# Optimization experiments

Hardware: AMD Instinct MI355X
Metric: run time of the kernel (lower is better)

The kernel has to match this reference:

```python
import jax, jax.numpy as jnp
import numpy as np

K_TOP = 2
NUM_HEADS = 8
NOISE_EPS = 0.01
GATE_EPS = 1e-9
LOSS_COEF = 0.01


def _xavier(key, shape):
    fan_in, fan_out = shape[-2], shape[-1]
    lim = float(np.sqrt(6.0 / (fan_in + fan_out)))
    return jax.random.uniform(key, shape, jnp.float32, -lim, lim)


def setup_inputs():
    key = jax.random.key(0)
    ks = jax.random.split(key, 12)
    B, S, D, E = 32, 512, 512, 8
    return {
        "q": jax.random.normal(ks[0], (B, S, D), jnp.float32),
        "k": jax.random.normal(ks[1], (B, S, D), jnp.float32),
        "v": jax.random.normal(ks[2], (B, S, D), jnp.float32),
        "mask": jnp.ones((1, 1, S, S), jnp.int32),
        "w_gate": _xavier(ks[3], (D, E)),
        "w_noise": _xavier(ks[4], (D, E)),
        "Wq": _xavier(ks[5], (E, D, D)),
        "bq": jnp.zeros((E, D), jnp.float32),
        "Wk": _xavier(ks[6], (E, D, D)),
        "bk": jnp.zeros((E, D), jnp.float32),
        "Wv": _xavier(ks[7], (E, D, D)),
        "bv": jnp.zeros((E, D), jnp.float32),
        "Wo": _xavier(ks[8], (E, D, D)),
        "bo": jnp.zeros((E, D), jnp.float32),
    }


def _cv_squared(x):
    # torch .var() is unbiased (ddof=1)
    return jnp.var(x, ddof=1) / (jnp.mean(x) ** 2 + 1e-10)


def _moe_attention(q, k, v, mask, w_gate, w_noise, Wq, bq, Wk, bk, Wv, bv, Wo, bo):
    B, S, D = q.shape
    E = w_gate.shape[1]
    H = NUM_HEADS
    dh = D // H

    # x[x != x] = 0 (in-place nan scrub of q, used for gating AND as query)
    qc = jnp.where(jnp.isnan(q), jnp.zeros((), q.dtype), q)

    # noisy top-k gating; the python loop sum_i x[:,i,:] @ W == x.sum(1) @ W
    xs = qc.sum(axis=1)                                  # [B, D]
    clean_logits = xs @ w_gate                           # [B, E]
    raw_noise = xs @ w_noise
    noise_std = jax.nn.softplus(raw_noise) + NOISE_EPS   # train=True
    noise = jax.random.normal(jax.random.key(42), clean_logits.shape, clean_logits.dtype)
    noisy_logits = clean_logits + noise * noise_std

    top_logits, top_idx = jax.lax.top_k(noisy_logits, K_TOP + 1)  # [B, k+1]
    tk_logits = top_logits[:, :K_TOP]
    tk_idx = top_idx[:, :K_TOP]                          # [B, k]
    tk_gates = jax.nn.softmax(tk_logits, axis=1) + GATE_EPS
    gates = jnp.zeros((B, E), clean_logits.dtype).at[jnp.arange(B)[:, None], tk_idx].set(tk_gates)

    # load via prob-in-top-k (noisy_gating and k < num_experts)
    thr_in = top_logits[:, K_TOP][:, None]
    thr_out = top_logits[:, K_TOP - 1][:, None]
    is_in = noisy_logits > thr_in
    cdf = jax.scipy.stats.norm.cdf
    prob = jnp.where(is_in, cdf((clean_logits - thr_in) / noise_std),
                     cdf((clean_logits - thr_out) / noise_std))
    load = prob.sum(axis=0)
    importance = gates.sum(axis=0)
    loss = (_cv_squared(importance) + _cv_squared(load)) * LOSS_COEF

    # sparse dispatch == per (batch, slot) run the selected expert's MHA.
    # Gather expert weights per selected slot: [B, k, D, D].
    def proj(x, W, b):
        return jnp.einsum('bsd,bjdf->bjsf', x, W[tk_idx]) + b[tk_idx][:, :, None, :]

    Q = proj(qc, Wq, bq).reshape(B, K_TOP, S, H, dh)
    Kx = proj(k, Wk, bk).reshape(B, K_TOP, S, H, dh)
    V = proj(v, Wv, bv).reshape(B, K_TOP, S, H, dh)

    scale = jnp.asarray(1.0 / np.sqrt(dh), q.dtype)
    scores = jnp.einsum('bjqhd,bjkhd->bjhqk', Q, Kx) * scale   # [B,k,H,S,S]
    m = mask[:, None]                                          # [1,1,1,S,S]
    scores = jnp.where(m == 0, jnp.asarray(-1e9, scores.dtype), scores)
    attn = jax.nn.softmax(scores, axis=-1)
    ctx = jnp.einsum('bjhqk,bjkhd->bjqhd', attn, V).reshape(B, K_TOP, S, D)
    out_e = jnp.einsum('bjsd,bjdf->bjsf', ctx, Wo[tk_idx]) + bo[tk_idx][:, :, None, :]

    # combine: sum_j gate * exp(out), clamp zeros to eps, log
    combined = jnp.einsum('bj,bjsd->bsd', tk_gates, jnp.exp(out_e))
    eps = jnp.asarray(np.finfo(np.float64).eps, combined.dtype)
    combined = jnp.where(combined == 0, eps, combined)
    return jnp.log(combined), loss


def reference(q, k, v, mask, w_gate, w_noise, Wq, bq, Wk, bk, Wv, bv, Wo, bo):
    return _moe_attention(q, k, v, mask, w_gate, w_noise, Wq, bq, Wk, bk, Wv, bv, Wo, bo)
```

## Files before the change

### kernel.cpp

```cpp
#include <hip/hip_runtime.h>
#include <math.h>

typedef unsigned int u32;
typedef unsigned long long u64;
typedef unsigned short u16t;

#define SD   512
#define EE   8
#define DH   64
#define SDSQ (512*512)
#define LDSW 72

typedef __attribute__((ext_vector_type(8))) short bfrag8;
typedef __attribute__((ext_vector_type(4))) float f32x4;
typedef __attribute__((ext_vector_type(8))) unsigned short u16x8;

typedef const __attribute__((address_space(1))) void gas_void;
typedef __attribute__((address_space(3))) void las_void;

#define MFMA_B16(a,b,c) __builtin_amdgcn_mfma_f32_16x16x32_bf16((a),(b),(c),0,0,0)

__device__ __forceinline__ u32 rotl32(u32 x, int r){ return (x<<r)|(x>>(32-r)); }

__device__ __forceinline__ u16t bf_hi(float a){
  u32 x; __builtin_memcpy(&x,&a,4);
  u32 r = x + 0x7fffu + ((x>>16)&1u);
  return (u16t)(r>>16);
}
__device__ __forceinline__ float bf_f(u16t h){
  u32 x = ((u32)h)<<16; float f; __builtin_memcpy(&f,&x,4); return f;
}
__device__ __forceinline__ void split2(float a, u16t& h, u16t& l){
  h = bf_hi(a);
  l = bf_hi(a - bf_f(h));
}

__device__ __forceinline__ void gload16(const u16t* g, u16t* l){
  __builtin_amdgcn_global_load_lds((gas_void*)g, (las_void*)l, 16, 0, 0);
}

__device__ __forceinline__ void threefry_0_42(u32 x0, u32 x1, u32& o0, u32& o1){
  const u32 k0=0u, k1=42u;
  const u32 ks2 = k0 ^ k1 ^ 0x1BD11BDAu;
  const int R0[4]={13,15,26,6}, R1[4]={17,29,16,24};
  x0 += k0; x1 += k1;
  #pragma unroll
  for(int r=0;r<4;r++){ x0+=x1; x1=rotl32(x1,R0[r]); x1^=x0; }
  x0+=k1; x1+=ks2+1u;
  #pragma unroll
  for(int r=0;r<4;r++){ x0+=x1; x1=rotl32(x1,R1[r]); x1^=x0; }
  x0+=ks2; x1+=k0+2u;
  #pragma unroll
  for(int r=0;r<4;r++){ x0+=x1; x1=rotl32(x1,R0[r]); x1^=x0; }
  x0+=k0; x1+=k1+3u;
  #pragma unroll
  for(int r=0;r<4;r++){ x0+=x1; x1=rotl32(x1,R1[r]); x1^=x0; }
  x0+=k1; x1+=ks2+4u;
  #pragma unroll
  for(int r=0;r<4;r++){ x0+=x1; x1=rotl32(x1,R0[r]); x1^=x0; }
  x0+=ks2; x1+=k0+5u;
  o0 = x0; o1 = x1;
}

__device__ double erfinv64(double x){
  double w = -log((1.0 - x) * (1.0 + x));
  double p;
  if (w < 5.0){
    w = w - 2.5;
    p = 2.81022636e-08;
    p = 3.43273939e-07 + p*w;
    p = -3.5233877e-06 + p*w;
    p = -4.39150654e-06 + p*w;
    p = 0.00021858087  + p*w;
    p = -0.00125372503 + p*w;
    p = -0.00417768164 + p*w;
    p = 0.246640727    + p*w;
    p = 1.50140941     + p*w;
  } else {
    w = sqrt(w) - 3.0;
    p = -0.000200214257;
    p = 0.000100950558 + p*w;
    p = 0.00134934322  + p*w;
    p = -0.00367342844 + p*w;
    p = 0.00573950773  + p*w;
    p = -0.0076224613  + p*w;
    p = 0.00943887047  + p*w;
    p = 1.00167406     + p*w;
    p = 2.83297682     + p*w;
  }
  double r = p * x;
  #pragma unroll
  for (int it=0; it<2; ++it){
    double e = erf(r) - x;
    r -= e / (1.1283791670955126 * exp(-r*r));
  }
  return r;
}

__device__ double jax_noise_part32(int i){
  u32 o0, o1;
  threefry_0_42(0u, (u32)i, o0, o1);
  u32 bits = o0 ^ o1;
  u32 fb = (bits >> 9) | 0x3f800000u;
  float f; __builtin_memcpy(&f, &fb, 4);
  f -= 1.0f;
  u32 lob = 0xBF7FFFFFu;
  float lo; __builtin_memcpy(&lo, &lob, 4);
  float t = f * 2.0f;
  float u = t + lo;
  u = fmaxf(u, lo);
  return 1.4142135623730951 * erfinv64((double)u);
}

__global__ __launch_bounds__(256) void k_cvt_x(
  const float* __restrict__ src, u16t* __restrict__ dh, u16t* __restrict__ dl, int clean)
{
  const int n4 = 32*SDSQ/4;
  int i = blockIdx.x*256 + threadIdx.x;
  if (i >= n4) return;
  float4 r = ((const float4*)src)[i];
  float a[4] = {r.x, r.y, r.z, r.w};
  if (clean){
    #pragma unroll
    for (int u=0;u<4;u++) if (isnan(a[u])) a[u] = 0.f;
  }
  u16t h[4], l[4];
  #pragma unroll
  for (int u=0;u<4;u++) split2(a[u], h[u], l[u]);
  ((ushort4*)dh)[i] = make_ushort4(h[0],h[1],h[2],h[3]);
  ((ushort4*)dl)[i] = make_ushort4(l[0],l[1],l[2],l[3]);
}

__global__ __launch_bounds__(256) void k_cvt_w(
  const float* __restrict__ W, u16t* __restrict__ th, u16t* __restrict__ tl)
{
  __shared__ u16t Th[64*LDSW], Tl[64*LDSW];
  int e = blockIdx.z;
  int k0 = blockIdx.y*64, f0 = blockIdx.x*64;
  int tid = threadIdx.x;
  int r = tid>>2, c4 = (tid&3)*16;
  const float* Wp = W + (size_t)e*SDSQ + (size_t)(k0+r)*SD + f0 + c4;
  #pragma unroll
  for (int i=0;i<4;i++){
    float4 rv = *(const float4*)(Wp + 4*i);
    float a[4]={rv.x,rv.y,rv.z,rv.w};
    #pragma unroll
    for (int u=0;u<4;u++){
      u16t h,l; split2(a[u],h,l);
      Th[(c4+4*i+u)*LDSW + r] = h;
      Tl[(c4+4*i+u)*LDSW + r] = l;
    }
  }
  __syncthreads();
  u16t* dh = th + (size_t)e*SDSQ + (size_t)(f0+r)*SD + k0 + c4;
  u16t* dl = tl + (size_t)e*SDSQ + (size_t)(f0+r)*SD + k0 + c4;
  *(u16x8*)dh     = *(const u16x8*)&Th[r*LDSW + c4];
  *(u16x8*)(dh+8) = *(const u16x8*)&Th[r*LDSW + c4 + 8];
  *(u16x8*)dl     = *(const u16x8*)&Tl[r*LDSW + c4];
  *(u16x8*)(dl+8) = *(const u16x8*)&Tl[r*LDSW + c4 + 8];
}

__global__ void k_xs(const float* __restrict__ q, double* __restrict__ xs){
  int b = blockIdx.x, d = threadIdx.x;
  const float* p = q + (size_t)b*SDSQ + d;
  double acc = 0.0;
  for (int s=0; s<SD; ++s){
    float f = p[(size_t)s*SD];
    if (!isnan(f)) acc += (double)f;
  }
  xs[b*SD + d] = acc;
}

__global__ __launch_bounds__(256) void k_gate(
    const double* __restrict__ xs, const float* __restrict__ wg,
    const float* __restrict__ wn, int* __restrict__ tk_idx,
    float* __restrict__ tk_gates, float* __restrict__ out_loss)
{
  __shared__ double cl_s[256], sd_s[256], nz_s[256], pr_s[256];
  __shared__ double thrI_s[32], thrO_s[32], g0_s[32], g1_s[32];
  __shared__ int i0_s[32], i1_s[32];
  int tid = threadIdx.x;
  int b = tid >> 3, e = tid & 7;
  double c=0.0, n=0.0;
  const double* xr = xs + b*SD;
  for (int d=0; d<SD; ++d){
    double x = xr[d];
    c += x * (double)wg[d*EE + e];
    n += x * (double)wn[d*EE + e];
  }
  double sp = fmax(n, 0.0) + log1p(exp(-fabs(n)));
  double sdv = sp + 0.01;
  double nz = c + jax_noise_part32(tid) * sdv;
  cl_s[tid]=c; sd_s[tid]=sdv; nz_s[tid]=nz;
  __syncthreads();
  if (tid < 32){
    int bb = tid;
    double v0=-INFINITY,v1=-INFINITY,v2=-INFINITY; int i0=0,i1=0;
    for (int ee=0; ee<8; ++ee){
      double vv = nz_s[bb*8+ee];
      if (vv > v0){ v2=v1; v1=v0;i1=i0; v0=vv;i0=ee; }
      else if (vv > v1){ v2=v1; v1=vv;i1=ee; }
      else if (vv > v2){ v2=vv; }
    }
    double e1 = exp(v1 - v0);
    double s = 1.0 + e1;
    double g0 = 1.0/s + 1e-9, g1 = e1/s + 1e-9;
    tk_idx[bb*2+0]=i0; tk_idx[bb*2+1]=i1;
    tk_gates[bb*2+0]=(float)g0; tk_gates[bb*2+1]=(float)g1;
    i0_s[bb]=i0; i1_s[bb]=i1; g0_s[bb]=g0; g1_s[bb]=g1;
    thrI_s[bb]=v2; thrO_s[bb]=v1;
  }
  __syncthreads();
  {
    double thrI = thrI_s[b], thrO = thrO_s[b];
    bool isin = nz_s[tid] > thrI;
    double t = (cl_s[tid] - (isin ? thrI : thrO)) / sd_s[tid];
    pr_s[tid] = 0.5 * (1.0 + erf(t * 0.7071067811865476));
  }
  __syncthreads();
  if (tid == 0){
    double imp[8], ld[8];
    for (int i=0;i<8;i++){ imp[i]=0.0; ld[i]=0.0; }
    for (int bb=0; bb<32; ++bb){
      imp[i0_s[bb]] += g0_s[bb];
      imp[i1_s[bb]] += g1_s[bb];
    }
    for (int i=0;i<256;i++) ld[i&7] += pr_s[i];
    double loss = 0.0;
    for (int a=0;a<2;a++){
      double* arr = a ? ld : imp;
      double mu=0.0; for(int i=0;i<8;i++) mu += arr[i]; mu *= 0.125;
      double var=0.0; for(int i=0;i<8;i++){ double dd=arr[i]-mu; var += dd*dd; }
      var *= (1.0/7.0);
      loss += var / (mu*mu + 1e-10);
    }
    loss *= 0.01;
    out_loss[0] = (float)loss;
  }
}

__global__ __launch_bounds__(256) void k_proj(
  const u16t* __restrict__ qh, const u16t* __restrict__ ql,
  const u16t* __restrict__ kh, const u16t* __restrict__ kl,
  const u16t* __restrict__ vh, const u16t* __restrict__ vl,
  const u16t* __restrict__ wqh, const u16t* __restrict__ wql,
  const u16t* __restrict__ wkh, const u16t* __restrict__ wkl,
  const u16t* __restrict__ wvh, const u16t* __restrict__ wvl,
  const float* __restrict__ bq, const float* __restrict__ bk, const float* __restrict__ bv,
  const int* __restrict__ tk_idx, int pair0,
  u16t* __restrict__ Qh, u16t* __restrict__ Ql,
  u16t* __restrict__ Kh, u16t* __restrict__ Kl,
  u16t* __restrict__ Vth, u16t* __restrict__ Vtl)
{
  __shared__ __align__(16) u16t SM[4*128*64];
  int z = blockIdx.z;
  int lp = z/3, m = z - lp*3;
  int gp = pair0 + lp;
  int b = gp >> 1;
  int e = tk_idx[gp] & 7;
  const u16t *Xh, *Xl, *Wh, *Wl; const float* bias; u16t *Yh, *Yl;
  if (m==0){ Xh=qh; Xl=ql; Wh=wqh; Wl=wql; bias=bq; Yh=Qh;  Yl=Ql;  }
  else if (m==1){ Xh=kh; Xl=kl; Wh=wkh; Wl=wkl; bias=bk; Yh=Kh;  Yl=Kl;  }
  else { Xh=vh; Xl=vl; Wh=wvh; Wl=wvl; bias=bv; Yh=Vth; Yl=Vtl; }
  bool tr = (m==2);
  Xh += (size_t)b*SDSQ; Xl += (size_t)b*SDSQ;
  Wh += (size_t)e*SDSQ; Wl += (size_t)e*SDSQ;
  bias += e*SD;
  Yh += (size_t)lp*SDSQ; Yl += (size_t)lp*SDSQ;

  int tid = threadIdx.x, w = tid>>6, lane = tid&63;
  int q16 = lane&15, quad = lane>>4;
  int wm = w>>1, wnn = w&1;
  int s0 = blockIdx.y*128, f0 = blockIdx.x*128;
  int row8 = lane>>3, cc = lane&7;
  int soff = (cc ^ row8)*8;
  int sw = q16 & 7;
  int aH_off = tr ? 16384 : 0;
  int bH_off = tr ? 0 : 16384;

  f32x4 acc[4][4];
  #pragma unroll
  for (int i=0;i<4;i++)
    #pragma unroll
    for (int j=0;j<4;j++) acc[i][j] = (f32x4){0.f,0.f,0.f,0.f};

  for (int k0=0;k0<SD;k0+=64){
    #pragma unroll
    for (int t=0;t<4;t++){
      int br = w*32 + t*8;
      int gr = br + row8;
      size_t ga  = (size_t)(s0+gr)*SD + k0 + soff;
      size_t gbo = (size_t)(f0+gr)*SD + k0 + soff;
      gload16(Xh + ga,  &SM[0     + br*64]);
      gload16(Xl + ga,  &SM[8192  + br*64]);
      gload16(Wh + gbo, &SM[16384 + br*64]);
      gload16(Wl + gbo, &SM[24576 + br*64]);
    }
    __syncthreads();
    #pragma unroll
    for (int kk=0;kk<2;kk++){
      int ch = kk*4 + quad;
      int co = (ch ^ sw)*8;
      bfrag8 fAH[4], fAL[4], fBH[4], fBL[4];
      #pragma unroll
      for (int i=0;i<4;i++){
        int ra = wm*64  + i*16 + q16;
        int rb = wnn*64 + i*16 + q16;
        fAH[i] = *(const bfrag8*)&SM[aH_off        + ra*64 + co];
        fAL[i] = *(const bfrag8*)&SM[aH_off + 8192 + ra*64 + co];
        fBH[i] = *(const bfrag8*)&SM[bH_off        + rb*64 + co];
        fBL[i] = *(const bfrag8*)&SM[bH_off + 8192 + rb*64 + co];
      }
      #pragma unroll
      for (int i=0;i<4;i++)
        #pragma unroll
        for (int j=0;j<4;j++){
          acc[i][j] = MFMA_B16(fAH[i], fBH[j], acc[i][j]);
          acc[i][j] = MFMA_B16(fAH[i], fBL[j], acc[i][j]);
          acc[i][j] = MFMA_B16(fAL[i], fBH[j], acc[i][j]);
        }
    }
    __syncthreads();
  }
  if (!tr){
    #pragma unroll
    for (int i=0;i<4;i++){
      #pragma unroll
      for (int j=0;j<4;j++){
        int f = f0 + wnn*64 + j*16 + q16;
        float bb = bias[f];
        #pragma unroll
        for (int rr=0;rr<4;rr++){
          int s = s0 + wm*64 + i*16 + quad*4 + rr;
          u16t hh, ll; split2(acc[i][j][rr] + bb, hh, ll);
          size_t o = (size_t)s*SD + f;
          Yh[o] = hh; Yl[o] = ll;
        }
      }
    }
  } else {
    #pragma unroll
    for (int i=0;i<4;i++){
      #pragma unroll
      for (int rr=0;rr<4;rr++){
        int fr = f0 + wm*64 + i*16 + quad*4 + rr;
        float bb = bias[fr];
        #pragma unroll
        for (int j=0;j<4;j++){
          int scol = s0 + wnn*64 + j*16 + q16;
          u16t hh, ll; split2(acc[i][j][rr] + bb, hh, ll);
          size_t o = (size_t)fr*SD + scol;
          Yh[o] = hh; Yl[o] = ll;
        }
      }
    }
  }
}

__global__ __launch_bounds__(256) void k_attn(
  const u16t* __restrict__ Qh, const u16t* __restrict__ Ql,
  const u16t* __restrict__ Kh, const u16t* __restrict__ Kl,
  const u16t* __restrict__ Vth, const u16t* __restrict__ Vtl,
  u16t* __restrict__ Ch, u16t* __restrict__ Cl)
{
  __shared__ __align__(16) u16t QH[64*64], QL[64*64];
  __shared__ __align__(16) u16t KH[64*64], KL[64*64];
  __shared__ __align__(16) u16t VTH[64*64], VTL[64*64];
  __shared__ __align__(16) u16t PS[64*LDSW];
  int lp = blockIdx.z, h = blockIdx.y, qt = blockIdx.x;
  int tid = threadIdx.x;
  int w = tid>>6, lane = tid&63, q16 = lane&15, quad = lane>>4;
  int s0 = qt*64;
  const size_t base  = (size_t)lp*SDSQ + h*DH;
  const size_t vbase = (size_t)lp*SDSQ + (size_t)h*DH*SD;
  int row8 = lane>>3, cc = lane&7;
  int soff = (cc ^ row8)*8;
  int sw = q16 & 7;

  #pragma unroll
  for (int t=0;t<2;t++){
    int br = w*16 + t*8, gr = br + row8;
    size_t ga = base + (size_t)(s0+gr)*SD + soff;
    gload16(Qh + ga, &QH[br*64]);
    gload16(Ql + ga, &QL[br*64]);
  }

  float m_row[4], l_row[4];
  f32x4 ctx[4];
  #pragma unroll
  for (int rr=0;rr<4;rr++){ m_row[rr]=-INFINITY; l_row[rr]=0.f; }
  #pragma unroll
  for (int nt=0;nt<4;nt++) ctx[nt] = (f32x4){0.f,0.f,0.f,0.f};

  for (int kt=0; kt<8; ++kt){
    #pragma unroll
    for (int t=0;t<2;t++){
      int br = w*16 + t*8, gr = br + row8;
      size_t gk = base + (size_t)(kt*64+gr)*SD + soff;
      gload16(Kh + gk, &KH[br*64]);
      gload16(Kl + gk, &KL[br*64]);
      size_t gv = vbase + (size_t)gr*SD + kt*64 + soff;
      gload16(Vth + gv, &VTH[br*64]);
      gload16(Vtl + gv, &VTL[br*64]);
    }
    __syncthreads();

    f32x4 sc[4];
    #pragma unroll
    for (int nt=0;nt<4;nt++) sc[nt] = (f32x4){0.f,0.f,0.f,0.f};
    #pragma unroll
    for (int kk=0;kk<2;kk++){
      int co = ((kk*4+quad) ^ sw)*8;
      bfrag8 aH = *(const bfrag8*)&QH[(w*16+q16)*64 + co];
      bfrag8 aL = *(const bfrag8*)&QL[(w*16+q16)*64 + co];
      #pragma unroll
      for (int nt=0;nt<4;nt++){
        bfrag8 bH = *(const bfrag8*)&KH[(nt*16+q16)*64 + co];
        bfrag8 bL = *(const bfrag8*)&KL[(nt*16+q16)*64 + co];
        sc[nt] = MFMA_B16(aH,bH,sc[nt]);
        sc[nt] = MFMA_B16(aH,bL,sc[nt]);
        sc[nt] = MFMA_B16(aL,bH,sc[nt]);
      }
    }
    #pragma unroll
    for (int nt=0;nt<4;nt++)
      #pragma unroll
      for (int rr=0;rr<4;rr++) sc[nt][rr] *= 0.125f;

    float alpha[4];
    #pragma unroll
    for (int rr=0;rr<4;rr++){
      float mx = sc[0][rr];
      #pragma unroll
      for (int nt=1;nt<4;nt++) mx = fmaxf(mx, sc[nt][rr]);
      mx = fmaxf(mx, __shfl_xor(mx, 1));
      mx = fmaxf(mx, __shfl_xor(mx, 2));
      mx = fmaxf(mx, __shfl_xor(mx, 4));
      mx = fmaxf(mx, __shfl_xor(mx, 8));
      float nm = fmaxf(m_row[rr], mx);
      alpha[rr] = expf(m_row[rr] - nm);
      m_row[rr] = nm;
    }
    #pragma unroll
    for (int rr=0;rr<4;rr++){
      float S = 0.f;
      #pragma unroll
      for (int nt=0;nt<4;nt++){
        float p = expf(sc[nt][rr] - m_row[rr]);
        sc[nt][rr] = p;
        S += p;
      }
      S += __shfl_xor(S, 1);
      S += __shfl_xor(S, 2);
      S += __shfl_xor(S, 4);
      S += __shfl_xor(S, 8);
      l_row[rr] = l_row[rr]*alpha[rr] + S;
      #pragma unroll
      for (int nt=0;nt<4;nt++) ctx[nt][rr] *= alpha[rr];
    }
    #pragma unroll
    for (int nt=0;nt<4;nt++)
      #pragma unroll
      for (int rr=0;rr<4;rr++)
        PS[(w*16 + quad*4 + rr)*LDSW + nt*16 + q16] = bf_hi(sc[nt][rr]);
    __syncthreads();

    #pragma unroll
    for (int kk2=0;kk2<2;kk2++){
      bfrag8 aP = *(const bfrag8*)&PS[(w*16+q16)*LDSW + kk2*32 + quad*8];
      int co2 = ((kk2*4+quad) ^ sw)*8;
      #pragma unroll
      for (int nt=0;nt<4;nt++){
        bfrag8 vH = *(const bfrag8*)&VTH[(nt*16+q16)*64 + co2];
        bfrag8 vL = *(const bfrag8*)&VTL[(nt*16+q16)*64 + co2];
        ctx[nt] = MFMA_B16(aP,vH,ctx[nt]);
        ctx[nt] = MFMA_B16(aP,vL,ctx[nt]);
      }
    }
    __syncthreads();
  }
  #pragma unroll
  for (int rr=0;rr<4;rr++){
    float inv = 1.f / l_row[rr];
    #pragma unroll
    for (int nt=0;nt<4;nt++){
      int s = s0 + w*16 + quad*4 + rr;
      u16t hh, ll; split2(ctx[nt][rr]*inv, hh, ll);
      size_t o = base + (size_t)s*SD + nt*16 + q16;
      Ch[o] = hh; Cl[o] = ll;
    }
  }
}

__global__ __launch_bounds__(256) void k_out(
  const u16t* __restrict__ Ch, const u16t* __restrict__ Cl,
  const u16t* __restrict__ Wth, const u16t* __restrict__ Wtl,
  const float* __restrict__ bo, const int* __restrict__ tk_idx,
  const float* __restrict__ tk_gates, int pair0, float* __restrict__ out)
{
  __shared__ __align__(16) u16t Ah[64*64], Al[64*64];
  __shared__ __align__(16) u16t Bh[64*64], Bl[64*64];
  int lb = blockIdx.z;
  int gb = (pair0 >> 1) + lb;
  int tid = threadIdx.x;
  int w = tid>>6, lane = tid&63, q16 = lane&15, quad = lane>>4;
  int s0 = blockIdx.y*64, f0 = blockIdx.x*64;
  int row8 = lane>>3, cc = lane&7;
  int soff = (cc ^ row8)*8;
  int sw = q16 & 7;

  f32x4 acc2[2][4];
  #pragma unroll
  for (int j=0;j<2;j++)
    #pragma unroll
    for (int nt=0;nt<4;nt++) acc2[j][nt] = (f32x4){0.f,0.f,0.f,0.f};

  for (int j=0;j<2;++j){
    int e = tk_idx[pair0 + lb*2 + j] & 7;
    const u16t* AH = Ch + (size_t)(lb*2+j)*SDSQ;
    const u16t* AL = Cl + (size_t)(lb*2+j)*SDSQ;
    const u16t* WH = Wth + (size_t)e*SDSQ;
    const u16t* WL = Wtl + (size_t)e*SDSQ;
    for (int k0=0;k0<SD;k0+=64){
      #pragma unroll
      for (int t=0;t<2;t++){
        int br = w*16 + t*8, gr = br + row8;
        size_t ga  = (size_t)(s0+gr)*SD + k0 + soff;
        size_t gbo = (size_t)(f0+gr)*SD + k0 + soff;
        gload16(AH + ga,  &Ah[br*64]);
        gload16(AL + ga,  &Al[br*64]);
        gload16(WH + gbo, &Bh[br*64]);
        gload16(WL + gbo, &Bl[br*64]);
      }
      __syncthreads();
      #pragma unroll
      for (int kk=0;kk<2;kk++){
        int co = ((kk*4+quad) ^ sw)*8;
        bfrag8 aH = *(const bfrag8*)&Ah[(w*16+q16)*64 + co];
        bfrag8 aL = *(const bfrag8*)&Al[(w*16+q16)*64 + co];
        #pragma unroll
        for (int nt=0;nt<4;nt++){
          bfrag8 bH = *(const bfrag8*)&Bh[(nt*16+q16)*64 + co];
          bfrag8 bL = *(const bfrag8*)&Bl[(nt*16+q16)*64 + co];
          acc2[j][nt] = MFMA_B16(aH,bH,acc2[j][nt]);
          acc2[j][nt] = MFMA_B16(aH,bL,acc2[j][nt]);
          acc2[j][nt] = MFMA_B16(aL,bH,acc2[j][nt]);
        }
      }
      __syncthreads();
    }
  }
  int e0 = tk_idx[pair0 + lb*2 + 0] & 7, e1 = tk_idx[pair0 + lb*2 + 1] & 7;
  float g0 = tk_gates[pair0 + lb*2 + 0], g1 = tk_gates[pair0 + lb*2 + 1];
  #pragma unroll
  for (int nt=0;nt<4;nt++){
    #pragma unroll
    for (int rr=0;rr<4;rr++){
      int s = s0 + w*16 + quad*4 + rr;
      int f = f0 + nt*16 + q16;
      float o0 = acc2[0][nt][rr] + bo[e0*SD+f];
      float o1 = acc2[1][nt][rr] + bo[e1*SD+f];
      float cmb = g0*expf(o0) + g1*expf(o1);
      if (cmb == 0.f) cmb = 2.2204460492503131e-16f;
      out[(size_t)gb*SDSQ + (size_t)s*SD + f] = logf(cmb);
    }
  }
}

extern "C" void kernel_launch(void* const* d_in, const int* in_sizes, int n_in,
                              void* d_out, int out_size, void* d_ws, size_t ws_size,
                              hipStream_t stream)
{
  const float* q  = (const float*)d_in[0];
  const float* k  = (const float*)d_in[1];
  const float* v  = (const float*)d_in[2];
  const float* wg = (const float*)d_in[4];
  const float* wn = (const float*)d_in[5];
  const float* Wq = (const float*)d_in[6];
  const float* bq = (const float*)d_in[7];
  const float* Wk = (const float*)d_in[8];
  const float* bk = (const float*)d_in[9];
  const float* Wv = (const float*)d_in[10];
  const float* bv = (const float*)d_in[11];
  const float* Wo = (const float*)d_in[12];
  const float* bo = (const float*)d_in[13];
  float* out = (float*)d_out;

  char* ws = (char*)d_ws;
  double* xs      = (double*)(ws + 0);
  int*   tk_idx   = (int*)  (ws + 131072);
  float* tk_gates = (float*)(ws + 131072 + 256);

  const size_t header = (size_t)1 << 20;
  const size_t XSB = (size_t)32 * SDSQ * 2;
  const size_t WSB = (size_t)8  * SDSQ * 2;
  u16t* qch = (u16t*)(ws + header + 0*XSB);
  u16t* qcl = (u16t*)(ws + header + 1*XSB);
  u16t* kh_ = (u16t*)(ws + header + 2*XSB);
  u16t* kl_ = (u16t*)(ws + header + 3*XSB);
  u16t* vh_ = (u16t*)(ws + header + 4*XSB);
  u16t* vl_ = (u16t*)(ws + header + 5*XSB);
  char* wbase = ws + header + 6*XSB;
  u16t* wqh = (u16t*)(wbase + 0*WSB);
  u16t* wql = (u16t*)(wbase + 1*WSB);
  u16t* wkh = (u16t*)(wbase + 2*WSB);
  u16t* wkl = (u16t*)(wbase + 3*WSB);
  u16t* wvh = (u16t*)(wbase + 4*WSB);
  u16t* wvl = (u16t*)(wbase + 5*WSB);
  u16t* woh = (u16t*)(wbase + 6*WSB);
  u16t* wol = (u16t*)(wbase + 7*WSB);
  char* bufbase = wbase + 8*WSB;

  const size_t slab = (size_t)SDSQ * 2;
  size_t used = (size_t)(bufbase - ws);
  size_t avail = (ws_size > used) ? (ws_size - used) : 0;
  int CH = (int)(avail / (6 * slab));
  CH &= ~1;
  if (CH > 64) CH = 64;
  if (CH < 2)  CH = 2;

  k_cvt_x<<<dim3(8192), dim3(256), 0, stream>>>(q, qch, qcl, 1);
  k_cvt_x<<<dim3(8192), dim3(256), 0, stream>>>(k, kh_, kl_, 0);
  k_cvt_x<<<dim3(8192), dim3(256), 0, stream>>>(v, vh_, vl_, 0);
  k_cvt_w<<<dim3(8,8,8), dim3(256), 0, stream>>>(Wq, wqh, wql);
  k_cvt_w<<<dim3(8,8,8), dim3(256), 0, stream>>>(Wk, wkh, wkl);
  k_cvt_w<<<dim3(8,8,8), dim3(256), 0, stream>>>(Wv, wvh, wvl);
  k_cvt_w<<<dim3(8,8,8), dim3(256), 0, stream>>>(Wo, woh, wol);

  k_xs  <<<dim3(32), dim3(512), 0, stream>>>(q, xs);
  k_gate<<<dim3(1), dim3(256), 0, stream>>>(xs, wg, wn, tk_idx, tk_gates,
                                            out + (size_t)out_size - 1);

  for (int pair0 = 0; pair0 < 64; pair0 += CH){
    int cur = (64 - pair0 < CH) ? (64 - pair0) : CH;
    u16t* Qh  = (u16t*)bufbase;
    u16t* Ql  = Qh  + (size_t)CH * SDSQ;
    u16t* Kh  = Ql  + (size_t)CH * SDSQ;
    u16t* Kl  = Kh  + (size_t)CH * SDSQ;
    u16t* Vth = Kl  + (size_t)CH * SDSQ;
    u16t* Vtl = Vth + (size_t)CH * SDSQ;
    u16t* Ch = Qh;
    u16t* Cl = Ql;

    k_proj<<<dim3(4,4,cur*3), dim3(256), 0, stream>>>(
        qch,qcl, kh_,kl_, vh_,vl_, wqh,wql, wkh,wkl, wvh,wvl,
        bq,bk,bv, tk_idx, pair0, Qh,Ql, Kh,Kl, Vth,Vtl);
    k_attn<<<dim3(8,8,cur), dim3(256), 0, stream>>>(Qh,Ql, Kh,Kl, Vth,Vtl, Ch,Cl);
    k_out <<<dim3(8,8,cur/2), dim3(256), 0, stream>>>(Ch,Cl, woh,wol, bo, tk_idx, tk_gates,
                                                      pair0, out);
  }
}
```

Baseline: 801.7 us.

## Remap blocks for XCD-local L2 reuse and slim attention LDS usage

All three kernels remap the flat block index so that consecutive logical tiles sharing the same inputs land on the same XCD. This follows the round-robin dispatch across the eight chiplets, so reused weights and K/V tiles can stay in one L2. The attention kernel now keeps Q fragments in registers instead of LDS and drops one __syncthreads by writing the probability tile with a swizzled layout. It also merges all shared buffers into a single smaller array and adds an occupancy hint of 4 blocks per CU. The remapping assumes the block count is divisible by 8 and that grid dimensions match the hard-coded decode shifts. The occupancy hint may increase register pressure.

```diff
diff --git a/kernel.cpp b/kernel.cpp
--- a/kernel.cpp
+++ b/kernel.cpp
@@ -253,7 +253,10 @@
   u16t* __restrict__ Vth, u16t* __restrict__ Vtl)
 {
   __shared__ __align__(16) u16t SM[4*128*64];
-  int z = blockIdx.z;
+  int Nb = gridDim.x*gridDim.y*gridDim.z;
+  int flat = blockIdx.x + gridDim.x*(blockIdx.y + gridDim.y*blockIdx.z);
+  int nf = (flat & 7)*(Nb>>3) + (flat>>3);
+  int bxx = nf & 3, byy = (nf>>2) & 3, z = nf >> 4;
   int lp = z/3, m = z - lp*3;
   int gp = pair0 + lp;
   int b = gp >> 1;
@@ -271,7 +274,7 @@
   int tid = threadIdx.x, w = tid>>6, lane = tid&63;
   int q16 = lane&15, quad = lane>>4;
   int wm = w>>1, wnn = w&1;
-  int s0 = blockIdx.y*128, f0 = blockIdx.x*128;
+  int s0 = byy*128, f0 = bxx*128;
   int row8 = lane>>3, cc = lane&7;
   int soff = (cc ^ row8)*8;
   int sw = q16 & 7;
@@ -357,19 +360,19 @@
   }
 }
 
-__global__ __launch_bounds__(256) void k_attn(
+__global__ __launch_bounds__(256, 4) void k_attn(
   const u16t* __restrict__ Qh, const u16t* __restrict__ Ql,
   const u16t* __restrict__ Kh, const u16t* __restrict__ Kl,
   const u16t* __restrict__ Vth, const u16t* __restrict__ Vtl,
   u16t* __restrict__ Ch, u16t* __restrict__ Cl)
 {
-  __shared__ __align__(16) u16t QH[64*64], QL[64*64];
-  __shared__ __align__(16) u16t KH[64*64], KL[64*64];
-  __shared__ __align__(16) u16t VTH[64*64], VTL[64*64];
-  __shared__ __align__(16) u16t PS[64*LDSW];
-  int lp = blockIdx.z, h = blockIdx.y, qt = blockIdx.x;
+  __shared__ __align__(16) u16t SM[20480];
   int tid = threadIdx.x;
   int w = tid>>6, lane = tid&63, q16 = lane&15, quad = lane>>4;
+  int Nb = gridDim.x*gridDim.y*gridDim.z;
+  int flat = blockIdx.x + gridDim.x*(blockIdx.y + gridDim.y*blockIdx.z);
+  int nf = (flat & 7)*(Nb>>3) + (flat>>3);
+  int qt = nf & 7, h = (nf>>3) & 7, lp = nf >> 6;
   int s0 = qt*64;
   const size_t base  = (size_t)lp*SDSQ + h*DH;
   const size_t vbase = (size_t)lp*SDSQ + (size_t)h*DH*SD;
@@ -377,12 +380,14 @@
   int soff = (cc ^ row8)*8;
   int sw = q16 & 7;
 
-  #pragma unroll
-  for (int t=0;t<2;t++){
-    int br = w*16 + t*8, gr = br + row8;
-    size_t ga = base + (size_t)(s0+gr)*SD + soff;
-    gload16(Qh + ga, &QH[br*64]);
-    gload16(Ql + ga, &QL[br*64]);
+  bfrag8 qH[2], qL[2];
+  {
+    const u16t* qp  = Qh + base + (size_t)(s0 + w*16 + q16)*SD + quad*8;
+    const u16t* qp2 = Ql + base + (size_t)(s0 + w*16 + q16)*SD + quad*8;
+    qH[0] = *(const bfrag8*)(qp);
+    qH[1] = *(const bfrag8*)(qp + 32);
+    qL[0] = *(const bfrag8*)(qp2);
+    qL[1] = *(const bfrag8*)(qp2 + 32);
   }
 
   float m_row[4], l_row[4];
@@ -395,13 +400,14 @@
   for (int kt=0; kt<8; ++kt){
     #pragma unroll
     for (int t=0;t<2;t++){
-      int br = w*16 + t*8, gr = br + row8;
+      int br = w*16 + t*8;
+      int gr = br + row8;
       size_t gk = base + (size_t)(kt*64+gr)*SD + soff;
-      gload16(Kh + gk, &KH[br*64]);
-      gload16(Kl + gk, &KL[br*64]);
+      gload16(Kh + gk, &SM[0    + br*64]);
+      gload16(Kl + gk, &SM[4096 + br*64]);
       size_t gv = vbase + (size_t)gr*SD + kt*64 + soff;
-      gload16(Vth + gv, &VTH[br*64]);
-      gload16(Vtl + gv, &VTL[br*64]);
+      gload16(Vth + gv, &SM[8192  + br*64]);
+      gload16(Vtl + gv, &SM[12288 + br*64]);
     }
     __syncthreads();
 
@@ -411,15 +417,13 @@
     #pragma unroll
     for (int kk=0;kk<2;kk++){
       int co = ((kk*4+quad) ^ sw)*8;
-      bfrag8 aH = *(const bfrag8*)&QH[(w*16+q16)*64 + co];
-      bfrag8 aL = *(const bfrag8*)&QL[(w*16+q16)*64 + co];
       #pragma unroll
       for (int nt=0;nt<4;nt++){
-        bfrag8 bH = *(const bfrag8*)&KH[(nt*16+q16)*64 + co];
-        bfrag8 bL = *(const bfrag8*)&KL[(nt*16+q16)*64 + co];
-        sc[nt] = MFMA_B16(aH,bH,sc[nt]);
-        sc[nt] = MFMA_B16(aH,bL,sc[nt]);
-        sc[nt] = MFMA_B16(aL,bH,sc[nt]);
+        bfrag8 bH = *(const bfrag8*)&SM[0    + (nt*16+q16)*64 + co];
+        bfrag8 bL = *(const bfrag8*)&SM[4096 + (nt*16+q16)*64 + co];
+        sc[nt] = MFMA_B16(qH[kk],bH,sc[nt]);
+        sc[nt] = MFMA_B16(qH[kk],bL,sc[nt]);
+        sc[nt] = MFMA_B16(qL[kk],bH,sc[nt]);
       }
     }
     #pragma unroll
@@ -459,20 +463,23 @@
       for (int nt=0;nt<4;nt++) ctx[nt][rr] *= alpha[rr];
     }
     #pragma unroll
-    for (int nt=0;nt<4;nt++)
-      #pragma unroll
-      for (int rr=0;rr<4;rr++)
-        PS[(w*16 + quad*4 + rr)*LDSW + nt*16 + q16] = bf_hi(sc[nt][rr]);
-    __syncthreads();
+    for (int nt=0;nt<4;nt++){
+      int c = nt*2 + (q16>>3);
+      #pragma unroll
+      for (int rr=0;rr<4;rr++){
+        int prow = quad*4 + rr;
+        SM[16384 + (w*16+prow)*64 + ((c ^ (prow&7))*8) + (q16&7)] = bf_hi(sc[nt][rr]);
+      }
+    }
 
     #pragma unroll
     for (int kk2=0;kk2<2;kk2++){
-      bfrag8 aP = *(const bfrag8*)&PS[(w*16+q16)*LDSW + kk2*32 + quad*8];
       int co2 = ((kk2*4+quad) ^ sw)*8;
+      bfrag8 aP = *(const bfrag8*)&SM[16384 + (w*16+q16)*64 + co2];
       #pragma unroll
       for (int nt=0;nt<4;nt++){
-        bfrag8 vH = *(const bfrag8*)&VTH[(nt*16+q16)*64 + co2];
-        bfrag8 vL = *(const bfrag8*)&VTL[(nt*16+q16)*64 + co2];
+        bfrag8 vH = *(const bfrag8*)&SM[8192  + (nt*16+q16)*64 + co2];
+        bfrag8 vL = *(const bfrag8*)&SM[12288 + (nt*16+q16)*64 + co2];
         ctx[nt] = MFMA_B16(aP,vH,ctx[nt]);
         ctx[nt] = MFMA_B16(aP,vL,ctx[nt]);
       }
@@ -500,11 +507,14 @@
 {
   __shared__ __align__(16) u16t Ah[64*64], Al[64*64];
   __shared__ __align__(16) u16t Bh[64*64], Bl[64*64];
-  int lb = blockIdx.z;
+  int Nb = gridDim.x*gridDim.y*gridDim.z;
+  int flat = blockIdx.x + gridDim.x*(blockIdx.y + gridDim.y*blockIdx.z);
+  int nf = (flat & 7)*(Nb>>3) + (flat>>3);
+  int bxx = nf & 7, byy = (nf>>3) & 7, lb = nf >> 6;
   int gb = (pair0 >> 1) + lb;
   int tid = threadIdx.x;
   int w = tid>>6, lane = tid&63, q16 = lane&15, quad = lane>>4;
-  int s0 = blockIdx.y*64, f0 = blockIdx.x*64;
+  int s0 = byy*64, f0 = bxx*64;
   int row8 = lane>>3, cc = lane&7;
   int soff = (cc ^ row8)*8;
   int sw = q16 & 7;
```

Result: faster. 761.7 us (-5.0%).
